# Kernel tuning notes

Measured on AMD Instinct MI355X. Metric: run time of the kernel, lower is better.

## Reference

```python
import jax, jax.numpy as jnp
import numpy as np

EPS = 1e-3  # keras LayerNormalization default epsilon

def layernorm(x, gamma, beta):
    mu = jnp.mean(x, axis=-1, keepdims=True)
    var = jnp.var(x, axis=-1, keepdims=True)
    return (x - mu) * jax.lax.rsqrt(var + EPS) * gamma + beta

def setup_inputs() -> dict:
    key = jax.random.key(0)
    ks = jax.random.split(key, 20)
    B, N, T, Dimg, H = 512, 100, 14, 2048, 768
    s = lambda k, *sh: jax.random.normal(k, sh, dtype=jnp.float32) * 0.02
    return {
        "img_feat": jax.random.normal(ks[0], (B, N, Dimg), dtype=jnp.float32),
        "ques_feat": jax.random.normal(ks[1], (B, T, H), dtype=jnp.float32),
        "Wc": s(ks[2], Dimg, H), "bc": jnp.zeros((H,), jnp.float32),
        "Wq": s(ks[3], H, H),    "bq": jnp.zeros((H,), jnp.float32),
        "Wi": s(ks[4], Dimg, H), "bi": jnp.zeros((H,), jnp.float32),
        "wqa": s(ks[5], H, 1), "bqa": jnp.zeros((1,), jnp.float32),
        "wia": s(ks[6], H, 1), "bia": jnp.zeros((1,), jnp.float32),
        "g1": jnp.ones((N,), jnp.float32), "b1": jnp.zeros((N,), jnp.float32),
        "g2": jnp.ones((H,), jnp.float32), "b2": jnp.zeros((H,), jnp.float32),
        "g3": jnp.ones((T,), jnp.float32), "b3": jnp.zeros((T,), jnp.float32),
        "g4": jnp.ones((H,), jnp.float32), "b4": jnp.zeros((H,), jnp.float32),
        "g5": jnp.ones((N,), jnp.float32), "b5": jnp.zeros((N,), jnp.float32),
    }

def reference(img_feat, ques_feat, Wc, bc, Wq, bq, Wi, bi, wqa, bqa, wia, bia,
              g1, b1, g2, b2, g3, b3, g4, b4, g5, b5):
    # img_feat: [B,N,Dimg], ques_feat: [B,T,H]
    img_corr = img_feat @ Wc + bc                                   # [B,N,H]
    wm = jnp.einsum('bth,bnh->btn', ques_feat, img_corr)            # [B,T,N]
    wm = jax.nn.relu(layernorm(wm, g1, b1))
    ques_embed = ques_feat @ Wq + bq                                # [B,T,H]
    img_embed = img_feat @ Wi + bi                                  # [B,N,H]
    transform_img = jnp.einsum('btn,bnh->bth', wm, img_embed)       # [B,T,H]
    ques_atten_sum = jax.nn.relu(layernorm(transform_img + ques_embed, g2, b2))
    # dropout is identity at inference
    ques_atten = (ques_atten_sum @ wqa + bqa)[..., 0]               # [B,T]
    ques_atten = jax.nn.softmax(layernorm(ques_atten, g3, b3), axis=-1)
    transform_ques = jnp.einsum('btn,bth->bnh', wm, ques_embed)     # [B,N,H]
    img_atten_sum = jax.nn.relu(layernorm(transform_ques + img_embed, g4, b4))
    img_atten = (img_atten_sum @ wia + bia)[..., 0]                 # [B,N]
    img_atten = jax.nn.softmax(layernorm(img_atten, g5, b5), axis=-1)
    ques_atten_feat = jnp.einsum('bt,bth->bh', ques_atten, ques_feat)  # [B,H]
    img_atten_feat = jnp.einsum('bn,bnd->bd', img_atten, img_feat)     # [B,Dimg]
    return (img_atten_feat, ques_atten_feat)
```

## Files before the change

### kernel.cpp

```cpp
#include <hip/hip_runtime.h>

using f32x4     = __attribute__((ext_vector_type(4))) float;
using bf16x8    = __attribute__((ext_vector_type(8))) short;
using ushort8_t = __attribute__((ext_vector_type(8))) unsigned short;

__device__ __forceinline__ unsigned short f2bf(float f) {
    unsigned u = __builtin_bit_cast(unsigned, f);
    u += 0x7fffu + ((u >> 16) & 1u);
    return (unsigned short)(u >> 16);
}
__device__ __forceinline__ float bf2f(unsigned short h) {
    return __builtin_bit_cast(float, (unsigned)h << 16);
}

__device__ __forceinline__ float wave_sum(float v) {
#pragma unroll
    for (int off = 32; off > 0; off >>= 1) v += __shfl_xor(v, off, 64);
    return v;
}
__device__ __forceinline__ float wave_max(float v) {
#pragma unroll
    for (int off = 32; off > 0; off >>= 1) v = fmaxf(v, __shfl_xor(v, off, 64));
    return v;
}

#define GLP(p)  ((const __attribute__((address_space(1))) void*)(p))
#define LDSP(p) ((__attribute__((address_space(3))) void*)(p))

__global__ __launch_bounds__(256) void cvt_bf16(const float* __restrict__ in,
                                                unsigned short* __restrict__ out, long n8) {
    long i = (long)blockIdx.x * 256 + threadIdx.x;
    long stride = (long)gridDim.x * 256;
    for (; i < n8; i += stride) {
        const float4* p = (const float4*)(in + i * 8);
        float4 a = p[0], b = p[1];
        ushort8_t v;
        v[0] = f2bf(a.x); v[1] = f2bf(a.y); v[2] = f2bf(a.z); v[3] = f2bf(a.w);
        v[4] = f2bf(b.x); v[5] = f2bf(b.y); v[6] = f2bf(b.z); v[7] = f2bf(b.w);
        *(ushort8_t*)(out + i * 8) = v;
    }
}

__global__ void pack_w(const float* __restrict__ Wc, const float* __restrict__ Wi,
                       unsigned short* __restrict__ Wp) {
    int n = blockIdx.x, k = blockIdx.y * 256 + threadIdx.x;
    float v = (n < 768) ? Wc[(size_t)k * 768 + n] : Wi[(size_t)k * 768 + (n - 768)];
    Wp[(size_t)n * 2048 + k] = f2bf(v);
}

__global__ void pack_wq(const float* __restrict__ Wq, unsigned short* __restrict__ Wqt) {
    int n = blockIdx.x, k = blockIdx.y * 256 + threadIdx.x;
    Wqt[(size_t)n * 768 + k] = f2bf(Wq[(size_t)k * 768 + n]);
}

template <int OUTBF>
__global__ __launch_bounds__(512, 1) void gemm8(
    const unsigned short* __restrict__ A, const unsigned short* __restrict__ Bt,
    const float* __restrict__ bias0, const float* __restrict__ bias1, int nsplit,
    void* __restrict__ Cv, int N, int K, int NTN)
{
    __shared__ unsigned short LA[2][2][8192];
    __shared__ unsigned short LB[2][2][8192];
    const int tid = threadIdx.x, lane = tid & 63, wid = tid >> 6;

    int nwg = (int)gridDim.x, bid = (int)blockIdx.x;
    if ((nwg & 7) == 0) { int cpx = nwg >> 3; bid = (bid & 7) * cpx + (bid >> 3); }
    const int tn = bid % NTN, tm = bid / NTN;
    const size_t m0 = (size_t)tm * 256, n0 = (size_t)tn * 256;
    const int NT = K >> 6;
    const int NIT = NT >> 1;

    const int wr = wid >> 2, wc = wid & 3;
    const int hb = wc >> 1;
    const int fr = lane & 15, fs = lane >> 4;

    const int r0 = tid >> 3, s0 = ((tid & 7) - r0) & 7;
    const int r1 = r0 + 64,  s1 = ((tid & 7) - r1) & 7;
    const unsigned short* pA[2][2];
    const unsigned short* pB[2][2];
#pragma unroll
    for (int h = 0; h < 2; ++h) {
        pA[h][0] = A  + (m0 + h * 128 + r0) * K + s0 * 8;
        pA[h][1] = A  + (m0 + h * 128 + r1) * K + s1 * 8;
        pB[h][0] = Bt + (n0 + h * 128 + r0) * K + s0 * 8;
        pB[h][1] = Bt + (n0 + h * 128 + r1) * K + s1 * 8;
    }
    const int d0 = tid * 8, d1 = (tid + 512) * 8;

#define STG_A(h, t, B_) do { \
    __builtin_amdgcn_global_load_lds(GLP(pA[h][0] + (size_t)(t) * 64), LDSP(&LA[B_][h][d0]), 16, 0, 0); \
    __builtin_amdgcn_global_load_lds(GLP(pA[h][1] + (size_t)(t) * 64), LDSP(&LA[B_][h][d1]), 16, 0, 0); \
} while (0)
#define STG_B(h, t, B_) do { \
    __builtin_amdgcn_global_load_lds(GLP(pB[h][0] + (size_t)(t) * 64), LDSP(&LB[B_][h][d0]), 16, 0, 0); \
    __builtin_amdgcn_global_load_lds(GLP(pB[h][1] + (size_t)(t) * 64), LDSP(&LB[B_][h][d1]), 16, 0, 0); \
} while (0)

    int offA[2][4], offB[2][2];
#pragma unroll
    for (int mq = 0; mq < 2; ++mq)
#pragma unroll
        for (int mfl = 0; mfl < 4; ++mfl) {
            int r = mq * 64 + mfl * 16 + fr;
            offA[mq][mfl] = r * 64 + ((fs + r) & 7) * 8;
        }
#pragma unroll
    for (int nq = 0; nq < 2; ++nq)
#pragma unroll
        for (int nfl = 0; nfl < 2; ++nfl) {
            int r = (wc & 1) * 64 + nq * 32 + nfl * 16 + fr;
            offB[nq][nfl] = r * 64 + ((fs + r) & 7) * 8;
        }

#define LDA_SUB(B_, mq) do { \
    _Pragma("unroll") \
    for (int mfl = 0; mfl < 4; ++mfl) { \
        av[mfl][0] = *(const bf16x8*)&LA[B_][wr][offA[mq][mfl]]; \
        av[mfl][1] = *(const bf16x8*)&LA[B_][wr][offA[mq][mfl] ^ 32]; \
    } } while (0)
#define LDB_SUB(B_, nq, bv) do { \
    _Pragma("unroll") \
    for (int nfl = 0; nfl < 2; ++nfl) { \
        bv[nfl][0] = *(const bf16x8*)&LB[B_][hb][offB[nq][nfl]]; \
        bv[nfl][1] = *(const bf16x8*)&LB[B_][hb][offB[nq][nfl] ^ 32]; \
    } } while (0)
#define MMA_Q(mq, nq, bv) do { \
    _Pragma("unroll") \
    for (int ks = 0; ks < 2; ++ks) \
    _Pragma("unroll") \
    for (int mfl = 0; mfl < 4; ++mfl) \
    _Pragma("unroll") \
    for (int nfl = 0; nfl < 2; ++nfl) \
        acc[mq * 4 + mfl][nq * 2 + nfl] = __builtin_amdgcn_mfma_f32_16x16x32_bf16( \
            av[mfl][ks], bv[nfl][ks], acc[mq * 4 + mfl][nq * 2 + nfl], 0, 0, 0); \
    } while (0)
#define BAR  __builtin_amdgcn_s_barrier()
#define SCB  __builtin_amdgcn_sched_barrier(0)
#define LGKM0 do { asm volatile("s_waitcnt lgkmcnt(0)" ::: "memory"); SCB; } while (0)
#define PRIO1 __builtin_amdgcn_s_setprio(1)
#define PRIO0 __builtin_amdgcn_s_setprio(0)

    f32x4 acc[8][4];
#pragma unroll
    for (int i = 0; i < 8; ++i)
#pragma unroll
        for (int j = 0; j < 4; ++j) acc[i][j] = (f32x4){0.f, 0.f, 0.f, 0.f};

    STG_A(0, 0, 0); STG_A(1, 0, 0); STG_B(0, 0, 0); STG_B(1, 0, 0);
    STG_B(0, 1, 1); STG_B(1, 1, 1);
    asm volatile("s_waitcnt vmcnt(4)" ::: "memory");
    SCB; BAR;

    for (int i = 0; i < NIT; ++i) {
        const int t0 = 2 * i, t1 = 2 * i + 1;
        const bool st = (t0 + 2 < NT);
        bf16x8 av[4][2], bv0[2][2], bv1[2][2];

        LDA_SUB(0, 0); LDB_SUB(0, 0, bv0);
        STG_A(0, t1, 1);
        SCB; BAR; LGKM0;
        PRIO1; MMA_Q(0, 0, bv0); PRIO0;
        BAR;
        LDB_SUB(0, 1, bv1);
        STG_A(1, t1, 1);
        SCB; BAR; LGKM0;
        PRIO1; MMA_Q(0, 1, bv1); PRIO0;
        BAR;
        LDA_SUB(0, 1);
        if (st) STG_B(0, t0 + 2, 0);
        SCB; BAR; LGKM0;
        PRIO1; MMA_Q(1, 1, bv1); PRIO0;
        BAR;
        if (st) STG_B(1, t0 + 2, 0);
        SCB; BAR;
        PRIO1; MMA_Q(1, 0, bv0); PRIO0;
        if (st) asm volatile("s_waitcnt vmcnt(4)" ::: "memory");
        else    asm volatile("s_waitcnt vmcnt(0)" ::: "memory");
        SCB; BAR;
        LDA_SUB(1, 0); LDB_SUB(1, 0, bv0);
        if (st) STG_A(0, t0 + 2, 0);
        SCB; BAR; LGKM0;
        PRIO1; MMA_Q(0, 0, bv0); PRIO0;
        BAR;
        LDB_SUB(1, 1, bv1);
        if (st) STG_A(1, t0 + 2, 0);
        SCB; BAR; LGKM0;
        PRIO1; MMA_Q(0, 1, bv1); PRIO0;
        BAR;
        LDA_SUB(1, 1);
        if (st) STG_B(0, t1 + 2, 1);
        SCB; BAR; LGKM0;
        PRIO1; MMA_Q(1, 1, bv1); PRIO0;
        BAR;
        if (st) STG_B(1, t1 + 2, 1);
        SCB; BAR;
        PRIO1; MMA_Q(1, 0, bv0); PRIO0;
        if (st) asm volatile("s_waitcnt vmcnt(4)" ::: "memory");
        else    asm volatile("s_waitcnt vmcnt(0)" ::: "memory");
        SCB; BAR;
    }

#undef STG_A
#undef STG_B
#undef LDA_SUB
#undef LDB_SUB
#undef MMA_Q
#undef BAR
#undef SCB
#undef LGKM0
#undef PRIO1
#undef PRIO0

    const int wm = wr * 128, wn = wc * 64;
#pragma unroll
    for (int nf = 0; nf < 4; ++nf) {
        int col = (int)n0 + wn + nf * 16 + fr;
        float bs = (col < nsplit) ? bias0[col] : bias1[col - nsplit];
#pragma unroll
        for (int mf = 0; mf < 8; ++mf) {
            size_t rowb = m0 + wm + mf * 16 + fs * 4;
#pragma unroll
            for (int r = 0; r < 4; ++r) {
                float v = acc[mf][nf][r] + bs;
                if (OUTBF) ((unsigned short*)Cv)[(rowb + r) * N + col] = f2bf(v);
                else       ((float*)Cv)[(rowb + r) * N + col] = v;
            }
        }
    }
}

__global__ __launch_bounds__(256) void wm_kernel(
    const unsigned short* __restrict__ qbf, const unsigned short* __restrict__ imgCE,
    const float* __restrict__ g1, const float* __restrict__ b1,
    float* __restrict__ wm_g)
{
    const int b = blockIdx.x, tid = threadIdx.x, lane = tid & 63, wid = tid >> 6;
    __shared__ float qf[14 * 768];
    __shared__ float wmr[14][100];

    const ushort8_t* src = (const ushort8_t*)(qbf + (size_t)b * 14 * 768);
    for (int i = tid; i < 14 * 768 / 8; i += 256) {
        ushort8_t v = src[i];
#pragma unroll
        for (int j = 0; j < 8; ++j) qf[i * 8 + j] = bf2f(v[j]);
    }
    __syncthreads();

    for (int n = wid; n < 100; n += 4) {
        const unsigned short* row = imgCE + ((size_t)b * 100 + n) * 1536;
        float r[12];
#pragma unroll
        for (int j = 0; j < 12; ++j) r[j] = bf2f(row[lane + 64 * j]);
        for (int t = 0; t < 14; ++t) {
            const float* q = qf + t * 768;
            float s = 0.f;
#pragma unroll
            for (int j = 0; j < 12; ++j) s = fmaf(r[j], q[lane + 64 * j], s);
            s = wave_sum(s);
            if (lane == 0) wmr[t][n] = s;
        }
    }
    __syncthreads();

    for (int t = wid; t < 14; t += 4) {
        float x0 = wmr[t][lane];
        float x1 = (lane + 64 < 100) ? wmr[t][lane + 64] : 0.f;
        float s = wave_sum(x0 + x1);
        float q = wave_sum(x0 * x0 + x1 * x1);
        float mu = s * (1.f / 100.f);
        float var = q * (1.f / 100.f) - mu * mu;
        float rs = rsqrtf(var + 1e-3f);
        float* dst = wm_g + ((size_t)b * 14 + t) * 100;
        {
            float v = (x0 - mu) * rs * g1[lane] + b1[lane];
            dst[lane] = v > 0.f ? v : 0.f;
        }
        if (lane + 64 < 100) {
            float v = (x1 - mu) * rs * g1[lane + 64] + b1[lane + 64];
            dst[lane + 64] = v > 0.f ? v : 0.f;
        }
    }
}

__global__ __launch_bounds__(256) void ques_kernel(
    const float* __restrict__ qf_g, const float* __restrict__ qe_g,
    const unsigned short* __restrict__ imgCE, const float* __restrict__ wm_g,
    const float* __restrict__ g2, const float* __restrict__ b2,
    const float* __restrict__ g3, const float* __restrict__ b3,
    const float* __restrict__ wqa, const float* __restrict__ bqa,
    float* __restrict__ out_q)
{
    const int b = blockIdx.x, tid = threadIdx.x, lane = tid & 63, wid = tid >> 6;
    __shared__ float qe[14 * 768];
    __shared__ float wm[14 * 100];
    __shared__ float red[4][28];
    __shared__ float mu_s[14], rs_s[14], qa_s[14], qw_s[14];

    {
        const float4* src = (const float4*)(qe_g + (size_t)b * 14 * 768);
        for (int i = tid; i < 14 * 768 / 4; i += 256) ((float4*)qe)[i] = src[i];
        const float* ws = wm_g + (size_t)b * 1400;
        for (int i = tid; i < 1400; i += 256) wm[i] = ws[i];
    }
    __syncthreads();

    float a0[14], a1[14], a2[14];
#pragma unroll
    for (int t = 0; t < 14; ++t) { a0[t] = 0.f; a1[t] = 0.f; a2[t] = 0.f; }

    const unsigned short* ie_base = imgCE + (size_t)b * 100 * 1536 + 768;
    for (int n = 0; n < 100; ++n) {
        const unsigned short* ie = ie_base + (size_t)n * 1536;
        float e0 = bf2f(ie[tid]), e1 = bf2f(ie[tid + 256]), e2 = bf2f(ie[tid + 512]);
#pragma unroll
        for (int t = 0; t < 14; ++t) {
            float w = wm[t * 100 + n];
            a0[t] = fmaf(w, e0, a0[t]); a1[t] = fmaf(w, e1, a1[t]); a2[t] = fmaf(w, e2, a2[t]);
        }
    }
#pragma unroll
    for (int t = 0; t < 14; ++t) {
        a0[t] += qe[t * 768 + tid];
        a1[t] += qe[t * 768 + tid + 256];
        a2[t] += qe[t * 768 + tid + 512];
    }
#pragma unroll
    for (int t = 0; t < 14; ++t) {
        float s = wave_sum(a0[t] + a1[t] + a2[t]);
        float q = wave_sum(a0[t] * a0[t] + a1[t] * a1[t] + a2[t] * a2[t]);
        if (lane == 0) { red[wid][t] = s; red[wid][14 + t] = q; }
    }
    __syncthreads();
    if (tid < 14) {
        float s = red[0][tid] + red[1][tid] + red[2][tid] + red[3][tid];
        float q = red[0][14 + tid] + red[1][14 + tid] + red[2][14 + tid] + red[3][14 + tid];
        float mu = s * (1.f / 768.f);
        float var = q * (1.f / 768.f) - mu * mu;
        mu_s[tid] = mu; rs_s[tid] = rsqrtf(var + 1e-3f);
    }
    __syncthreads();

    float ga = g2[tid], ba = b2[tid], gb = g2[tid + 256], bb = b2[tid + 256],
          gc = g2[tid + 512], bc_ = b2[tid + 512];
    float w0 = wqa[tid], w1 = wqa[tid + 256], w2 = wqa[tid + 512];
#pragma unroll
    for (int t = 0; t < 14; ++t) {
        float mu = mu_s[t], rs = rs_s[t];
        float v0 = fmaxf((a0[t] - mu) * rs * ga + ba, 0.f);
        float v1 = fmaxf((a1[t] - mu) * rs * gb + bb, 0.f);
        float v2 = fmaxf((a2[t] - mu) * rs * gc + bc_, 0.f);
        float p = wave_sum(v0 * w0 + v1 * w1 + v2 * w2);
        if (lane == 0) red[wid][t] = p;
    }
    __syncthreads();
    if (tid < 14) qa_s[tid] = red[0][tid] + red[1][tid] + red[2][tid] + red[3][tid] + bqa[0];
    __syncthreads();
    if (tid == 0) {
        float s = 0.f;
        for (int t = 0; t < 14; ++t) s += qa_s[t];
        float mu = s * (1.f / 14.f);
        float q = 0.f;
        for (int t = 0; t < 14; ++t) { float d = qa_s[t] - mu; q += d * d; }
        float rs = rsqrtf(q * (1.f / 14.f) + 1e-3f);
        float e[14], mx = -1e30f;
        for (int t = 0; t < 14; ++t) { e[t] = (qa_s[t] - mu) * rs * g3[t] + b3[t]; mx = fmaxf(mx, e[t]); }
        float se = 0.f;
        for (int t = 0; t < 14; ++t) { e[t] = expf(e[t] - mx); se += e[t]; }
        float inv = 1.f / se;
        for (int t = 0; t < 14; ++t) qw_s[t] = e[t] * inv;
    }
    __syncthreads();

    const float* qf = qf_g + (size_t)b * 14 * 768;
#pragma unroll
    for (int c = 0; c < 3; ++c) {
        int h = tid + c * 256;
        float o = 0.f;
#pragma unroll
        for (int t = 0; t < 14; ++t) o = fmaf(qw_s[t], qf[t * 768 + h], o);
        out_q[(size_t)b * 768 + h] = o;
    }
}

__global__ __launch_bounds__(256) void img_kernel(
    const unsigned short* __restrict__ imf_bf, const float* __restrict__ qe_g,
    const unsigned short* __restrict__ imgCE, const float* __restrict__ wm_g,
    const float* __restrict__ g4, const float* __restrict__ b4,
    const float* __restrict__ g5, const float* __restrict__ b5,
    const float* __restrict__ wia, const float* __restrict__ bia,
    float* __restrict__ out_i)
{
    const int b = blockIdx.x, tid = threadIdx.x, lane = tid & 63, wid = tid >> 6;
    __shared__ float qe[14 * 768];
    __shared__ float wm[14 * 100];
    __shared__ float red[4][20];
    __shared__ float mu_s[10], rs_s[10];
    __shared__ float ia_s[100], iw_s[100];

    {
        const float4* src = (const float4*)(qe_g + (size_t)b * 14 * 768);
        for (int i = tid; i < 14 * 768 / 4; i += 256) ((float4*)qe)[i] = src[i];
        const float* ws = wm_g + (size_t)b * 1400;
        for (int i = tid; i < 1400; i += 256) wm[i] = ws[i];
    }
    __syncthreads();

    float g4a = g4[tid], b4a = b4[tid], g4b = g4[tid + 256], b4b = b4[tid + 256],
          g4c = g4[tid + 512], b4c = b4[tid + 512];
    float wa = wia[tid], wb = wia[tid + 256], wc_ = wia[tid + 512];

    for (int g = 0; g < 10; ++g) {
        float t0[10], t1[10], t2[10];
#pragma unroll
        for (int i = 0; i < 10; ++i) { t0[i] = 0.f; t1[i] = 0.f; t2[i] = 0.f; }
#pragma unroll
        for (int t = 0; t < 14; ++t) {
            float q0 = qe[t * 768 + tid], q1 = qe[t * 768 + tid + 256], q2 = qe[t * 768 + tid + 512];
#pragma unroll
            for (int i = 0; i < 10; ++i) {
                float w = wm[t * 100 + g * 10 + i];
                t0[i] = fmaf(w, q0, t0[i]); t1[i] = fmaf(w, q1, t1[i]); t2[i] = fmaf(w, q2, t2[i]);
            }
        }
#pragma unroll
        for (int i = 0; i < 10; ++i) {
            const unsigned short* ie = imgCE + ((size_t)b * 100 + g * 10 + i) * 1536 + 768;
            t0[i] += bf2f(ie[tid]); t1[i] += bf2f(ie[tid + 256]); t2[i] += bf2f(ie[tid + 512]);
            float s = wave_sum(t0[i] + t1[i] + t2[i]);
            float q = wave_sum(t0[i] * t0[i] + t1[i] * t1[i] + t2[i] * t2[i]);
            if (lane == 0) { red[wid][i] = s; red[wid][10 + i] = q; }
        }
        __syncthreads();
        if (tid < 10) {
            float s = red[0][tid] + red[1][tid] + red[2][tid] + red[3][tid];
            float q = red[0][10 + tid] + red[1][10 + tid] + red[2][10 + tid] + red[3][10 + tid];
            float mu = s * (1.f / 768.f);
            float var = q * (1.f / 768.f) - mu * mu;
            mu_s[tid] = mu; rs_s[tid] = rsqrtf(var + 1e-3f);
        }
        __syncthreads();
#pragma unroll
        for (int i = 0; i < 10; ++i) {
            float mu = mu_s[i], rs = rs_s[i];
            float v0 = fmaxf((t0[i] - mu) * rs * g4a + b4a, 0.f);
            float v1 = fmaxf((t1[i] - mu) * rs * g4b + b4b, 0.f);
            float v2 = fmaxf((t2[i] - mu) * rs * g4c + b4c, 0.f);
            float p = wave_sum(v0 * wa + v1 * wb + v2 * wc_);
            if (lane == 0) red[wid][i] = p;
        }
        __syncthreads();
        if (tid < 10) ia_s[g * 10 + tid] = red[0][tid] + red[1][tid] + red[2][tid] + red[3][tid] + bia[0];
        __syncthreads();
    }

    if (wid == 0) {
        float x0 = ia_s[lane];
        float x1 = (lane + 64 < 100) ? ia_s[lane + 64] : 0.f;
        float s = wave_sum(x0 + x1);
        float q = wave_sum(x0 * x0 + x1 * x1);
        float mu = s * 0.01f;
        float var = q * 0.01f - mu * mu;
        float rs = rsqrtf(var + 1e-3f);
        float v0 = (x0 - mu) * rs * g5[lane] + b5[lane];
        float v1 = (lane + 64 < 100) ? (x1 - mu) * rs * g5[lane + 64] + b5[lane + 64] : -1e30f;
        float mx = wave_max(fmaxf(v0, v1));
        float e0 = expf(v0 - mx);
        float e1 = (lane + 64 < 100) ? expf(v1 - mx) : 0.f;
        float se = wave_sum(e0 + e1);
        float inv = 1.f / se;
        iw_s[lane] = e0 * inv;
        if (lane + 64 < 100) iw_s[lane + 64] = e1 * inv;
    }
    __syncthreads();

    const unsigned short* imf = imf_bf + (size_t)b * 100 * 2048;
    float acc8[8];
#pragma unroll
    for (int j = 0; j < 8; ++j) acc8[j] = 0.f;
    for (int n = 0; n < 100; ++n) {
        ushort8_t v = *(const ushort8_t*)(imf + (size_t)n * 2048 + tid * 8);
        float w = iw_s[n];
#pragma unroll
        for (int j = 0; j < 8; ++j) acc8[j] = fmaf(w, bf2f(v[j]), acc8[j]);
    }
    float4* dst = (float4*)(out_i + (size_t)b * 2048);
    float4 oA = {acc8[0], acc8[1], acc8[2], acc8[3]};
    float4 oB = {acc8[4], acc8[5], acc8[6], acc8[7]};
    dst[tid * 2] = oA; dst[tid * 2 + 1] = oB;
}

extern "C" void kernel_launch(void* const* d_in, const int* in_sizes, int n_in,
                              void* d_out, int out_size, void* d_ws, size_t ws_size,
                              hipStream_t stream)
{
    const float* img_feat = (const float*)d_in[0];
    const float* ques_feat = (const float*)d_in[1];
    const float* Wc = (const float*)d_in[2];
    const float* bc = (const float*)d_in[3];
    const float* Wq = (const float*)d_in[4];
    const float* bq = (const float*)d_in[5];
    const float* Wi = (const float*)d_in[6];
    const float* bi = (const float*)d_in[7];
    const float* wqa = (const float*)d_in[8];
    const float* bqa = (const float*)d_in[9];
    const float* wia = (const float*)d_in[10];
    const float* bia = (const float*)d_in[11];
    const float* g1 = (const float*)d_in[12]; const float* b1 = (const float*)d_in[13];
    const float* g2 = (const float*)d_in[14]; const float* b2 = (const float*)d_in[15];
    const float* g3 = (const float*)d_in[16]; const float* b3 = (const float*)d_in[17];
    const float* g4 = (const float*)d_in[18]; const float* b4 = (const float*)d_in[19];
    const float* g5 = (const float*)d_in[20]; const float* b5 = (const float*)d_in[21];

    const size_t SZ_WP   = 1536u * 2048u * 2u;
    const size_t SZ_WQT  = 768u * 768u * 2u;
    const size_t SZ_IMG  = 51200ull * 1536u * 2u;
    const size_t SZ_QE   = 7168u * 768u * 4u;
    const size_t SZ_WM   = 512u * 1400u * 4u;
    const size_t SZ_ABF  = 51200ull * 2048u * 2u;
    const size_t SZ_QBF  = 7168u * 768u * 2u;

    const size_t OFF_WP  = 0;
    const size_t OFF_WQT = OFF_WP + SZ_WP;
    const size_t OFF_IMG = OFF_WQT + SZ_WQT;
    const size_t OFF_QE  = OFF_IMG + SZ_IMG;
    const size_t OFF_WM  = OFF_QE + SZ_QE;
    const size_t OFF_ABF = OFF_WM + SZ_WM;
    const size_t OFF_QBF = OFF_ABF + SZ_ABF;
    const size_t NEED    = OFF_QBF + SZ_QBF;
    if (ws_size < NEED) return;

    char* ws = (char*)d_ws;
    unsigned short* Wp    = (unsigned short*)(ws + OFF_WP);
    unsigned short* Wqt   = (unsigned short*)(ws + OFF_WQT);
    unsigned short* imgCE = (unsigned short*)(ws + OFF_IMG);
    float*          qe    = (float*)(ws + OFF_QE);
    float*          wm    = (float*)(ws + OFF_WM);
    unsigned short* Abf   = (unsigned short*)(ws + OFF_ABF);
    unsigned short* Qbf   = (unsigned short*)(ws + OFF_QBF);

    float* out_img = (float*)d_out;
    float* out_q   = (float*)d_out + 512 * 2048;

    hipLaunchKernelGGL(pack_w,  dim3(1536, 8), dim3(256), 0, stream, Wc, Wi, Wp);
    hipLaunchKernelGGL(pack_wq, dim3(768, 3),  dim3(256), 0, stream, Wq, Wqt);
    hipLaunchKernelGGL(cvt_bf16, dim3(2048), dim3(256), 0, stream,
                       img_feat, Abf, (long)(51200ull * 2048u / 8u));
    hipLaunchKernelGGL(cvt_bf16, dim3(1024), dim3(256), 0, stream,
                       ques_feat, Qbf, (long)(7168u * 768u / 8u));

    hipLaunchKernelGGL(HIP_KERNEL_NAME(gemm8<1>), dim3(1200), dim3(512), 0, stream,
                       Abf, Wp, bc, bi, 768, (void*)imgCE, 1536, 2048, 6);
    hipLaunchKernelGGL(HIP_KERNEL_NAME(gemm8<0>), dim3(84), dim3(512), 0, stream,
                       Qbf, Wqt, bq, bq, 768, (void*)qe, 768, 768, 3);

    hipLaunchKernelGGL(wm_kernel, dim3(512), dim3(256), 0, stream,
                       Qbf, imgCE, g1, b1, wm);
    hipLaunchKernelGGL(ques_kernel, dim3(512), dim3(256), 0, stream,
                       ques_feat, qe, imgCE, wm, g2, b2, g3, b3, wqa, bqa, out_q);
    hipLaunchKernelGGL(img_kernel, dim3(512), dim3(256), 0, stream,
                       Abf, qe, imgCE, wm, g4, b4, g5, b5, wia, bia, out_img);
}
```

Baseline: 798.8 us.

## Fuse attention-stage kernels into one per-batch kernel and rebalance GEMM prefetch

Merges the three per-batch kernels (wm, ques, img) into a single kernel that keeps the normalized wm matrix and the question embedding in shared memory. This drops the global wm round-trip, one reload of qe, and two launches. The GEMM main loop also moves global-to-LDS staging earlier (one more A subtile in flight, waitcnt raised from 4 to 6) and removes some sched barriers, giving more load/MMA overlap. The cost is that the fused kernel runs its ques and img phases one after the other in each block, so the two can no longer overlap across launches, and the deeper prefetch must still be correct against LDS buffer reuse.

```diff
diff --git a/kernel.cpp b/kernel.cpp
--- a/kernel.cpp
+++ b/kernel.cpp
@@ -147,55 +147,53 @@
         for (int j = 0; j < 4; ++j) acc[i][j] = (f32x4){0.f, 0.f, 0.f, 0.f};
 
     STG_A(0, 0, 0); STG_A(1, 0, 0); STG_B(0, 0, 0); STG_B(1, 0, 0);
-    STG_B(0, 1, 1); STG_B(1, 1, 1);
-    asm volatile("s_waitcnt vmcnt(4)" ::: "memory");
+    STG_B(0, 1, 1); STG_B(1, 1, 1); STG_A(0, 1, 1);
+    asm volatile("s_waitcnt vmcnt(6)" ::: "memory");
     SCB; BAR;
 
     for (int i = 0; i < NIT; ++i) {
         const int t0 = 2 * i, t1 = 2 * i + 1;
-        const bool st = (t0 + 2 < NT);
+        const bool st = (i + 1 < NIT);
         bf16x8 av[4][2], bv0[2][2], bv1[2][2];
 
         LDA_SUB(0, 0); LDB_SUB(0, 0, bv0);
-        STG_A(0, t1, 1);
-        SCB; BAR; LGKM0;
+        STG_A(1, t1, 1);
+        BAR; LGKM0;
         PRIO1; MMA_Q(0, 0, bv0); PRIO0;
         BAR;
         LDB_SUB(0, 1, bv1);
-        STG_A(1, t1, 1);
-        SCB; BAR; LGKM0;
+        BAR; LGKM0;
         PRIO1; MMA_Q(0, 1, bv1); PRIO0;
         BAR;
         LDA_SUB(0, 1);
         if (st) STG_B(0, t0 + 2, 0);
-        SCB; BAR; LGKM0;
+        BAR; LGKM0;
         PRIO1; MMA_Q(1, 1, bv1); PRIO0;
         BAR;
-        if (st) STG_B(1, t0 + 2, 0);
-        SCB; BAR;
+        if (st) { STG_B(1, t0 + 2, 0); STG_A(0, t0 + 2, 0); }
+        BAR;
         PRIO1; MMA_Q(1, 0, bv0); PRIO0;
-        if (st) asm volatile("s_waitcnt vmcnt(4)" ::: "memory");
+        if (st) asm volatile("s_waitcnt vmcnt(6)" ::: "memory");
         else    asm volatile("s_waitcnt vmcnt(0)" ::: "memory");
         SCB; BAR;
         LDA_SUB(1, 0); LDB_SUB(1, 0, bv0);
-        if (st) STG_A(0, t0 + 2, 0);
-        SCB; BAR; LGKM0;
+        if (st) STG_A(1, t0 + 2, 0);
+        BAR; LGKM0;
         PRIO1; MMA_Q(0, 0, bv0); PRIO0;
         BAR;
         LDB_SUB(1, 1, bv1);
-        if (st) STG_A(1, t0 + 2, 0);
-        SCB; BAR; LGKM0;
+        BAR; LGKM0;
         PRIO1; MMA_Q(0, 1, bv1); PRIO0;
         BAR;
         LDA_SUB(1, 1);
         if (st) STG_B(0, t1 + 2, 1);
-        SCB; BAR; LGKM0;
+        BAR; LGKM0;
         PRIO1; MMA_Q(1, 1, bv1); PRIO0;
         BAR;
-        if (st) STG_B(1, t1 + 2, 1);
-        SCB; BAR;
+        if (st) { STG_B(1, t1 + 2, 1); STG_A(0, t1 + 2, 1); }
+        BAR;
         PRIO1; MMA_Q(1, 0, bv0); PRIO0;
-        if (st) asm volatile("s_waitcnt vmcnt(4)" ::: "memory");
+        if (st) asm volatile("s_waitcnt vmcnt(6)" ::: "memory");
         else    asm volatile("s_waitcnt vmcnt(0)" ::: "memory");
         SCB; BAR;
     }
@@ -229,264 +227,238 @@
     }
 }
 
-__global__ __launch_bounds__(256) void wm_kernel(
-    const unsigned short* __restrict__ qbf, const unsigned short* __restrict__ imgCE,
+__global__ __launch_bounds__(256) void fused_kernel(
+    const float* __restrict__ qf_g, const unsigned short* __restrict__ qbf,
+    const float* __restrict__ qe_g, const unsigned short* __restrict__ imgCE,
+    const unsigned short* __restrict__ imf_bf,
     const float* __restrict__ g1, const float* __restrict__ b1,
-    float* __restrict__ wm_g)
+    const float* __restrict__ g2, const float* __restrict__ b2,
+    const float* __restrict__ g3, const float* __restrict__ b3,
+    const float* __restrict__ g4, const float* __restrict__ b4,
+    const float* __restrict__ g5, const float* __restrict__ b5,
+    const float* __restrict__ wqa, const float* __restrict__ bqa,
+    const float* __restrict__ wia, const float* __restrict__ bia,
+    float* __restrict__ out_i, float* __restrict__ out_q)
 {
     const int b = blockIdx.x, tid = threadIdx.x, lane = tid & 63, wid = tid >> 6;
-    __shared__ float qf[14 * 768];
-    __shared__ float wmr[14][100];
-
-    const ushort8_t* src = (const ushort8_t*)(qbf + (size_t)b * 14 * 768);
-    for (int i = tid; i < 14 * 768 / 8; i += 256) {
-        ushort8_t v = src[i];
-#pragma unroll
-        for (int j = 0; j < 8; ++j) qf[i * 8 + j] = bf2f(v[j]);
+    __shared__ float buf[14 * 768];
+    __shared__ float wms[14 * 100];
+    __shared__ float red[4][28];
+    __shared__ float mu_s[14], rs_s[14], qa_s[14], qw_s[14];
+    __shared__ float mu2_s[10], rs2_s[10];
+    __shared__ float ia_s[100], iw_s[100];
+
+    {
+        const ushort8_t* src = (const ushort8_t*)(qbf + (size_t)b * 14 * 768);
+        for (int i = tid; i < 14 * 768 / 8; i += 256) {
+            ushort8_t v = src[i];
+#pragma unroll
+            for (int j = 0; j < 8; ++j) buf[i * 8 + j] = bf2f(v[j]);
+        }
     }
     __syncthreads();
-
     for (int n = wid; n < 100; n += 4) {
         const unsigned short* row = imgCE + ((size_t)b * 100 + n) * 1536;
         float r[12];
 #pragma unroll
         for (int j = 0; j < 12; ++j) r[j] = bf2f(row[lane + 64 * j]);
         for (int t = 0; t < 14; ++t) {
-            const float* q = qf + t * 768;
+            const float* q = buf + t * 768;
             float s = 0.f;
 #pragma unroll
             for (int j = 0; j < 12; ++j) s = fmaf(r[j], q[lane + 64 * j], s);
             s = wave_sum(s);
-            if (lane == 0) wmr[t][n] = s;
+            if (lane == 0) wms[t * 100 + n] = s;
         }
     }
     __syncthreads();
-
     for (int t = wid; t < 14; t += 4) {
-        float x0 = wmr[t][lane];
-        float x1 = (lane + 64 < 100) ? wmr[t][lane + 64] : 0.f;
+        float x0 = wms[t * 100 + lane];
+        float x1 = (lane + 64 < 100) ? wms[t * 100 + lane + 64] : 0.f;
         float s = wave_sum(x0 + x1);
         float q = wave_sum(x0 * x0 + x1 * x1);
         float mu = s * (1.f / 100.f);
         float var = q * (1.f / 100.f) - mu * mu;
         float rs = rsqrtf(var + 1e-3f);
-        float* dst = wm_g + ((size_t)b * 14 + t) * 100;
         {
             float v = (x0 - mu) * rs * g1[lane] + b1[lane];
-            dst[lane] = v > 0.f ? v : 0.f;
+            wms[t * 100 + lane] = v > 0.f ? v : 0.f;
         }
         if (lane + 64 < 100) {
             float v = (x1 - mu) * rs * g1[lane + 64] + b1[lane + 64];
-            dst[lane + 64] = v > 0.f ? v : 0.f;
-        }
-    }
-}
-
-__global__ __launch_bounds__(256) void ques_kernel(
-    const float* __restrict__ qf_g, const float* __restrict__ qe_g,
-    const unsigned short* __restrict__ imgCE, const float* __restrict__ wm_g,
-    const float* __restrict__ g2, const float* __restrict__ b2,
-    const float* __restrict__ g3, const float* __restrict__ b3,
-    const float* __restrict__ wqa, const float* __restrict__ bqa,
-    float* __restrict__ out_q)
-{
-    const int b = blockIdx.x, tid = threadIdx.x, lane = tid & 63, wid = tid >> 6;
-    __shared__ float qe[14 * 768];
-    __shared__ float wm[14 * 100];
-    __shared__ float red[4][28];
-    __shared__ float mu_s[14], rs_s[14], qa_s[14], qw_s[14];
-
+            wms[t * 100 + lane + 64] = v > 0.f ? v : 0.f;
+        }
+    }
     {
         const float4* src = (const float4*)(qe_g + (size_t)b * 14 * 768);
-        for (int i = tid; i < 14 * 768 / 4; i += 256) ((float4*)qe)[i] = src[i];
-        const float* ws = wm_g + (size_t)b * 1400;
-        for (int i = tid; i < 1400; i += 256) wm[i] = ws[i];
+        for (int i = tid; i < 14 * 768 / 4; i += 256) ((float4*)buf)[i] = src[i];
     }
     __syncthreads();
 
-    float a0[14], a1[14], a2[14];
-#pragma unroll
-    for (int t = 0; t < 14; ++t) { a0[t] = 0.f; a1[t] = 0.f; a2[t] = 0.f; }
-
-    const unsigned short* ie_base = imgCE + (size_t)b * 100 * 1536 + 768;
-    for (int n = 0; n < 100; ++n) {
-        const unsigned short* ie = ie_base + (size_t)n * 1536;
-        float e0 = bf2f(ie[tid]), e1 = bf2f(ie[tid + 256]), e2 = bf2f(ie[tid + 512]);
+    {
+        float a0[14], a1[14], a2[14];
+#pragma unroll
+        for (int t = 0; t < 14; ++t) { a0[t] = 0.f; a1[t] = 0.f; a2[t] = 0.f; }
+
+        const unsigned short* ie_base = imgCE + (size_t)b * 100 * 1536 + 768;
+        for (int n = 0; n < 100; ++n) {
+            const unsigned short* ie = ie_base + (size_t)n * 1536;
+            float e0 = bf2f(ie[tid]), e1 = bf2f(ie[tid + 256]), e2 = bf2f(ie[tid + 512]);
+#pragma unroll
+            for (int t = 0; t < 14; ++t) {
+                float w = wms[t * 100 + n];
+                a0[t] = fmaf(w, e0, a0[t]); a1[t] = fmaf(w, e1, a1[t]); a2[t] = fmaf(w, e2, a2[t]);
+            }
+        }
 #pragma unroll
         for (int t = 0; t < 14; ++t) {
-            float w = wm[t * 100 + n];
-            a0[t] = fmaf(w, e0, a0[t]); a1[t] = fmaf(w, e1, a1[t]); a2[t] = fmaf(w, e2, a2[t]);
-        }
-    }
-#pragma unroll
-    for (int t = 0; t < 14; ++t) {
-        a0[t] += qe[t * 768 + tid];
-        a1[t] += qe[t * 768 + tid + 256];
-        a2[t] += qe[t * 768 + tid + 512];
-    }
-#pragma unroll
-    for (int t = 0; t < 14; ++t) {
-        float s = wave_sum(a0[t] + a1[t] + a2[t]);
-        float q = wave_sum(a0[t] * a0[t] + a1[t] * a1[t] + a2[t] * a2[t]);
-        if (lane == 0) { red[wid][t] = s; red[wid][14 + t] = q; }
-    }
-    __syncthreads();
-    if (tid < 14) {
-        float s = red[0][tid] + red[1][tid] + red[2][tid] + red[3][tid];
-        float q = red[0][14 + tid] + red[1][14 + tid] + red[2][14 + tid] + red[3][14 + tid];
-        float mu = s * (1.f / 768.f);
-        float var = q * (1.f / 768.f) - mu * mu;
-        mu_s[tid] = mu; rs_s[tid] = rsqrtf(var + 1e-3f);
-    }
-    __syncthreads();
-
-    float ga = g2[tid], ba = b2[tid], gb = g2[tid + 256], bb = b2[tid + 256],
-          gc = g2[tid + 512], bc_ = b2[tid + 512];
-    float w0 = wqa[tid], w1 = wqa[tid + 256], w2 = wqa[tid + 512];
-#pragma unroll
-    for (int t = 0; t < 14; ++t) {
-        float mu = mu_s[t], rs = rs_s[t];
-        float v0 = fmaxf((a0[t] - mu) * rs * ga + ba, 0.f);
-        float v1 = fmaxf((a1[t] - mu) * rs * gb + bb, 0.f);
-        float v2 = fmaxf((a2[t] - mu) * rs * gc + bc_, 0.f);
-        float p = wave_sum(v0 * w0 + v1 * w1 + v2 * w2);
-        if (lane == 0) red[wid][t] = p;
-    }
-    __syncthreads();
-    if (tid < 14) qa_s[tid] = red[0][tid] + red[1][tid] + red[2][tid] + red[3][tid] + bqa[0];
-    __syncthreads();
-    if (tid == 0) {
-        float s = 0.f;
-        for (int t = 0; t < 14; ++t) s += qa_s[t];
-        float mu = s * (1.f / 14.f);
-        float q = 0.f;
-        for (int t = 0; t < 14; ++t) { float d = qa_s[t] - mu; q += d * d; }
-        float rs = rsqrtf(q * (1.f / 14.f) + 1e-3f);
-        float e[14], mx = -1e30f;
-        for (int t = 0; t < 14; ++t) { e[t] = (qa_s[t] - mu) * rs * g3[t] + b3[t]; mx = fmaxf(mx, e[t]); }
-        float se = 0.f;
-        for (int t = 0; t < 14; ++t) { e[t] = expf(e[t] - mx); se += e[t]; }
-        float inv = 1.f / se;
-        for (int t = 0; t < 14; ++t) qw_s[t] = e[t] * inv;
-    }
-    __syncthreads();
-
-    const float* qf = qf_g + (size_t)b * 14 * 768;
-#pragma unroll
-    for (int c = 0; c < 3; ++c) {
-        int h = tid + c * 256;
-        float o = 0.f;
-#pragma unroll
-        for (int t = 0; t < 14; ++t) o = fmaf(qw_s[t], qf[t * 768 + h], o);
-        out_q[(size_t)b * 768 + h] = o;
-    }
-}
-
-__global__ __launch_bounds__(256) void img_kernel(
-    const unsigned short* __restrict__ imf_bf, const float* __restrict__ qe_g,
-    const unsigned short* __restrict__ imgCE, const float* __restrict__ wm_g,
-    const float* __restrict__ g4, const float* __restrict__ b4,
-    const float* __restrict__ g5, const float* __restrict__ b5,
-    const float* __restrict__ wia, const float* __restrict__ bia,
-    float* __restrict__ out_i)
-{
-    const int b = blockIdx.x, tid = threadIdx.x, lane = tid & 63, wid = tid >> 6;
-    __shared__ float qe[14 * 768];
-    __shared__ float wm[14 * 100];
-    __shared__ float red[4][20];
-    __shared__ float mu_s[10], rs_s[10];
-    __shared__ float ia_s[100], iw_s[100];
-
-    {
-        const float4* src = (const float4*)(qe_g + (size_t)b * 14 * 768);
-        for (int i = tid; i < 14 * 768 / 4; i += 256) ((float4*)qe)[i] = src[i];
-        const float* ws = wm_g + (size_t)b * 1400;
-        for (int i = tid; i < 1400; i += 256) wm[i] = ws[i];
-    }
-    __syncthreads();
-
-    float g4a = g4[tid], b4a = b4[tid], g4b = g4[tid + 256], b4b = b4[tid + 256],
-          g4c = g4[tid + 512], b4c = b4[tid + 512];
-    float wa = wia[tid], wb = wia[tid + 256], wc_ = wia[tid + 512];
-
-    for (int g = 0; g < 10; ++g) {
-        float t0[10], t1[10], t2[10];
-#pragma unroll
-        for (int i = 0; i < 10; ++i) { t0[i] = 0.f; t1[i] = 0.f; t2[i] = 0.f; }
+            a0[t] += buf[t * 768 + tid];
+            a1[t] += buf[t * 768 + tid + 256];
+            a2[t] += buf[t * 768 + tid + 512];
+        }
 #pragma unroll
         for (int t = 0; t < 14; ++t) {
-            float q0 = qe[t * 768 + tid], q1 = qe[t * 768 + tid + 256], q2 = qe[t * 768 + tid + 512];
-#pragma unroll
-            for (int i = 0; i < 10; ++i) {
-                float w = wm[t * 100 + g * 10 + i];
-                t0[i] = fmaf(w, q0, t0[i]); t1[i] = fmaf(w, q1, t1[i]); t2[i] = fmaf(w, q2, t2[i]);
-            }
-        }
-#pragma unroll
-        for (int i = 0; i < 10; ++i) {
-            const unsigned short* ie = imgCE + ((size_t)b * 100 + g * 10 + i) * 1536 + 768;
-            t0[i] += bf2f(ie[tid]); t1[i] += bf2f(ie[tid + 256]); t2[i] += bf2f(ie[tid + 512]);
-            float s = wave_sum(t0[i] + t1[i] + t2[i]);
-            float q = wave_sum(t0[i] * t0[i] + t1[i] * t1[i] + t2[i] * t2[i]);
-            if (lane == 0) { red[wid][i] = s; red[wid][10 + i] = q; }
+            float s = wave_sum(a0[t] + a1[t] + a2[t]);
+            float q = wave_sum(a0[t] * a0[t] + a1[t] * a1[t] + a2[t] * a2[t]);
+            if (lane == 0) { red[wid][t] = s; red[wid][14 + t] = q; }
         }
         __syncthreads();
-        if (tid < 10) {
+        if (tid < 14) {
             float s = red[0][tid] + red[1][tid] + red[2][tid] + red[3][tid];
-            float q = red[0][10 + tid] + red[1][10 + tid] + red[2][10 + tid] + red[3][10 + tid];
+            float q = red[0][14 + tid] + red[1][14 + tid] + red[2][14 + tid] + red[3][14 + tid];
             float mu = s * (1.f / 768.f);
             float var = q * (1.f / 768.f) - mu * mu;
             mu_s[tid] = mu; rs_s[tid] = rsqrtf(var + 1e-3f);
         }
         __syncthreads();
-#pragma unroll
-        for (int i = 0; i < 10; ++i) {
-            float mu = mu_s[i], rs = rs_s[i];
-            float v0 = fmaxf((t0[i] - mu) * rs * g4a + b4a, 0.f);
-            float v1 = fmaxf((t1[i] - mu) * rs * g4b + b4b, 0.f);
-            float v2 = fmaxf((t2[i] - mu) * rs * g4c + b4c, 0.f);
-            float p = wave_sum(v0 * wa + v1 * wb + v2 * wc_);
-            if (lane == 0) red[wid][i] = p;
+
+        float ga = g2[tid], ba = b2[tid], gb = g2[tid + 256], bb = b2[tid + 256],
+              gc = g2[tid + 512], bc_ = b2[tid + 512];
+        float w0 = wqa[tid], w1 = wqa[tid + 256], w2 = wqa[tid + 512];
+#pragma unroll
+        for (int t = 0; t < 14; ++t) {
+            float mu = mu_s[t], rs = rs_s[t];
+            float v0 = fmaxf((a0[t] - mu) * rs * ga + ba, 0.f);
+            float v1 = fmaxf((a1[t] - mu) * rs * gb + bb, 0.f);
+            float v2 = fmaxf((a2[t] - mu) * rs * gc + bc_, 0.f);
+            float p = wave_sum(v0 * w0 + v1 * w1 + v2 * w2);
+            if (lane == 0) red[wid][t] = p;
         }
         __syncthreads();
-        if (tid < 10) ia_s[g * 10 + tid] = red[0][tid] + red[1][tid] + red[2][tid] + red[3][tid] + bia[0];
+        if (tid < 14) qa_s[tid] = red[0][tid] + red[1][tid] + red[2][tid] + red[3][tid] + bqa[0];
         __syncthreads();
-    }
-
-    if (wid == 0) {
-        float x0 = ia_s[lane];
-        float x1 = (lane + 64 < 100) ? ia_s[lane + 64] : 0.f;
-        float s = wave_sum(x0 + x1);
-        float q = wave_sum(x0 * x0 + x1 * x1);
-        float mu = s * 0.01f;
-        float var = q * 0.01f - mu * mu;
-        float rs = rsqrtf(var + 1e-3f);
-        float v0 = (x0 - mu) * rs * g5[lane] + b5[lane];
-        float v1 = (lane + 64 < 100) ? (x1 - mu) * rs * g5[lane + 64] + b5[lane + 64] : -1e30f;
-        float mx = wave_max(fmaxf(v0, v1));
-        float e0 = expf(v0 - mx);
-        float e1 = (lane + 64 < 100) ? expf(v1 - mx) : 0.f;
-        float se = wave_sum(e0 + e1);
-        float inv = 1.f / se;
-        iw_s[lane] = e0 * inv;
-        if (lane + 64 < 100) iw_s[lane + 64] = e1 * inv;
+        if (tid == 0) {
+            float s = 0.f;
+            for (int t = 0; t < 14; ++t) s += qa_s[t];
+            float mu = s * (1.f / 14.f);
+            float q = 0.f;
+            for (int t = 0; t < 14; ++t) { float d = qa_s[t] - mu; q += d * d; }
+            float rs = rsqrtf(q * (1.f / 14.f) + 1e-3f);
+            float e[14], mx = -1e30f;
+            for (int t = 0; t < 14; ++t) { e[t] = (qa_s[t] - mu) * rs * g3[t] + b3[t]; mx = fmaxf(mx, e[t]); }
+            float se = 0.f;
+            for (int t = 0; t < 14; ++t) { e[t] = expf(e[t] - mx); se += e[t]; }
+            float inv = 1.f / se;
+            for (int t = 0; t < 14; ++t) qw_s[t] = e[t] * inv;
+        }
+        __syncthreads();
+
+        const float* qf = qf_g + (size_t)b * 14 * 768;
+#pragma unroll
+        for (int c = 0; c < 3; ++c) {
+            int h = tid + c * 256;
+            float o = 0.f;
+#pragma unroll
+            for (int t = 0; t < 14; ++t) o = fmaf(qw_s[t], qf[t * 768 + h], o);
+            out_q[(size_t)b * 768 + h] = o;
+        }
     }
     __syncthreads();
 
-    const unsigned short* imf = imf_bf + (size_t)b * 100 * 2048;
-    float acc8[8];
-#pragma unroll
-    for (int j = 0; j < 8; ++j) acc8[j] = 0.f;
-    for (int n = 0; n < 100; ++n) {
-        ushort8_t v = *(const ushort8_t*)(imf + (size_t)n * 2048 + tid * 8);
-        float w = iw_s[n];
-#pragma unroll
-        for (int j = 0; j < 8; ++j) acc8[j] = fmaf(w, bf2f(v[j]), acc8[j]);
-    }
-    float4* dst = (float4*)(out_i + (size_t)b * 2048);
-    float4 oA = {acc8[0], acc8[1], acc8[2], acc8[3]};
-    float4 oB = {acc8[4], acc8[5], acc8[6], acc8[7]};
-    dst[tid * 2] = oA; dst[tid * 2 + 1] = oB;
+    {
+        float g4a = g4[tid], b4a = b4[tid], g4b = g4[tid + 256], b4b = b4[tid + 256],
+              g4c = g4[tid + 512], b4c = b4[tid + 512];
+        float wa = wia[tid], wb = wia[tid + 256], wc_ = wia[tid + 512];
+
+        for (int g = 0; g < 10; ++g) {
+            float t0[10], t1[10], t2[10];
+#pragma unroll
+            for (int i = 0; i < 10; ++i) { t0[i] = 0.f; t1[i] = 0.f; t2[i] = 0.f; }
+#pragma unroll
+            for (int t = 0; t < 14; ++t) {
+                float q0 = buf[t * 768 + tid], q1 = buf[t * 768 + tid + 256], q2 = buf[t * 768 + tid + 512];
+#pragma unroll
+                for (int i = 0; i < 10; ++i) {
+                    float w = wms[t * 100 + g * 10 + i];
+                    t0[i] = fmaf(w, q0, t0[i]); t1[i] = fmaf(w, q1, t1[i]); t2[i] = fmaf(w, q2, t2[i]);
+                }
+            }
+#pragma unroll
+            for (int i = 0; i < 10; ++i) {
+                const unsigned short* ie = imgCE + ((size_t)b * 100 + g * 10 + i) * 1536 + 768;
+                t0[i] += bf2f(ie[tid]); t1[i] += bf2f(ie[tid + 256]); t2[i] += bf2f(ie[tid + 512]);
+                float s = wave_sum(t0[i] + t1[i] + t2[i]);
+                float q = wave_sum(t0[i] * t0[i] + t1[i] * t1[i] + t2[i] * t2[i]);
+                if (lane == 0) { red[wid][i] = s; red[wid][10 + i] = q; }
+            }
+            __syncthreads();
+            if (tid < 10) {
+                float s = red[0][tid] + red[1][tid] + red[2][tid] + red[3][tid];
+                float q = red[0][10 + tid] + red[1][10 + tid] + red[2][10 + tid] + red[3][10 + tid];
+                float mu = s * (1.f / 768.f);
+                float var = q * (1.f / 768.f) - mu * mu;
+                mu2_s[tid] = mu; rs2_s[tid] = rsqrtf(var + 1e-3f);
+            }
+            __syncthreads();
+#pragma unroll
+            for (int i = 0; i < 10; ++i) {
+                float mu = mu2_s[i], rs = rs2_s[i];
+                float v0 = fmaxf((t0[i] - mu) * rs * g4a + b4a, 0.f);
+                float v1 = fmaxf((t1[i] - mu) * rs * g4b + b4b, 0.f);
+                float v2 = fmaxf((t2[i] - mu) * rs * g4c + b4c, 0.f);
+                float p = wave_sum(v0 * wa + v1 * wb + v2 * wc_);
+                if (lane == 0) red[wid][i] = p;
+            }
+            __syncthreads();
+            if (tid < 10) ia_s[g * 10 + tid] = red[0][tid] + red[1][tid] + red[2][tid] + red[3][tid] + bia[0];
+            __syncthreads();
+        }
+
+        if (wid == 0) {
+            float x0 = ia_s[lane];
+            float x1 = (lane + 64 < 100) ? ia_s[lane + 64] : 0.f;
+            float s = wave_sum(x0 + x1);
+            float q = wave_sum(x0 * x0 + x1 * x1);
+            float mu = s * 0.01f;
+            float var = q * 0.01f - mu * mu;
+            float rs = rsqrtf(var + 1e-3f);
+            float v0 = (x0 - mu) * rs * g5[lane] + b5[lane];
+            float v1 = (lane + 64 < 100) ? (x1 - mu) * rs * g5[lane + 64] + b5[lane + 64] : -1e30f;
+            float mx = wave_max(fmaxf(v0, v1));
+            float e0 = expf(v0 - mx);
+            float e1 = (lane + 64 < 100) ? expf(v1 - mx) : 0.f;
+            float se = wave_sum(e0 + e1);
+            float inv = 1.f / se;
+            iw_s[lane] = e0 * inv;
+            if (lane + 64 < 100) iw_s[lane + 64] = e1 * inv;
+        }
+        __syncthreads();
+
+        const unsigned short* imf = imf_bf + (size_t)b * 100 * 2048;
+        float acc8[8];
+#pragma unroll
+        for (int j = 0; j < 8; ++j) acc8[j] = 0.f;
+        for (int n = 0; n < 100; ++n) {
+            ushort8_t v = *(const ushort8_t*)(imf + (size_t)n * 2048 + tid * 8);
+            float w = iw_s[n];
+#pragma unroll
+            for (int j = 0; j < 8; ++j) acc8[j] = fmaf(w, bf2f(v[j]), acc8[j]);
+        }
+        float4* dst = (float4*)(out_i + (size_t)b * 2048);
+        float4 oA = {acc8[0], acc8[1], acc8[2], acc8[3]};
+        float4 oB = {acc8[4], acc8[5], acc8[6], acc8[7]};
+        dst[tid * 2] = oA; dst[tid * 2 + 1] = oB;
+    }
 }
 
 extern "C" void kernel_launch(void* const* d_in, const int* in_sizes, int n_in,
@@ -534,7 +506,6 @@
     unsigned short* Wqt   = (unsigned short*)(ws + OFF_WQT);
     unsigned short* imgCE = (unsigned short*)(ws + OFF_IMG);
     float*          qe    = (float*)(ws + OFF_QE);
-    float*          wm    = (float*)(ws + OFF_WM);
     unsigned short* Abf   = (unsigned short*)(ws + OFF_ABF);
     unsigned short* Qbf   = (unsigned short*)(ws + OFF_QBF);
 
@@ -553,10 +524,8 @@
     hipLaunchKernelGGL(HIP_KERNEL_NAME(gemm8<0>), dim3(84), dim3(512), 0, stream,
                        Qbf, Wqt, bq, bq, 768, (void*)qe, 768, 768, 3);
 
-    hipLaunchKernelGGL(wm_kernel, dim3(512), dim3(256), 0, stream,
-                       Qbf, imgCE, g1, b1, wm);
-    hipLaunchKernelGGL(ques_kernel, dim3(512), dim3(256), 0, stream,
-                       ques_feat, qe, imgCE, wm, g2, b2, g3, b3, wqa, bqa, out_q);
-    hipLaunchKernelGGL(img_kernel, dim3(512), dim3(256), 0, stream,
-                       Abf, qe, imgCE, wm, g4, b4, g5, b5, wia, bia, out_img);
-}
+    hipLaunchKernelGGL(fused_kernel, dim3(512), dim3(256), 0, stream,
+                       ques_feat, Qbf, qe, imgCE, Abf,
+                       g1, b1, g2, b2, g3, b3, g4, b4, g5, b5,
+                       wqa, bqa, wia, bia, out_img, out_q);
+}
```

After: 788.2 us. Within noise of the previous version (-1.3%).
